# Optimization experiments

Hardware: AMD Instinct MI355X
Metric: run time of the kernel (lower is better)

Reference implementation:

```python
import jax, jax.numpy as jnp
import numpy as np

ATTN, ENC, DEC = 1024, 1024, 1024
B, S = 64, 2048

def setup_inputs() -> dict:
    key = jax.random.key(0)
    k1, k2, k3, k4, k5, k6 = jax.random.split(key, 6)
    sc_w = 1.0 / np.sqrt(ENC + DEC)
    sc_v = 1.0 / np.sqrt(ATTN)
    return {
        "hidden": jax.random.normal(k1, (B, DEC), dtype=jnp.float32),
        "vectors_to_attend": jax.random.normal(k2, (S, B, ENC), dtype=jnp.float32),
        "attn_w_weight": jax.random.uniform(k3, (ATTN, ENC + DEC), jnp.float32, -sc_w, sc_w),
        "attn_w_bias": jax.random.uniform(k4, (ATTN,), jnp.float32, -sc_w, sc_w),
        "attn_v_weight": jax.random.uniform(k5, (1, ATTN), jnp.float32, -sc_v, sc_v),
        "attn_v_bias": jax.random.uniform(k6, (1,), jnp.float32, -sc_v, sc_v),
    }

def reference(hidden, vectors_to_attend, attn_w_weight, attn_w_bias, attn_v_weight, attn_v_bias):
    # vectors_to_attend: [S, B, E] -> [B, S, E]
    v = jnp.transpose(vectors_to_attend, (1, 0, 2))
    # Split attn_w over the concat dim: concat([v, h]) @ W^T == v @ We^T + h @ Wd^T
    We = attn_w_weight[:, :ENC]   # [A, E]
    Wd = attn_w_weight[:, ENC:]   # [A, D]
    # energies: [B, S, A]
    e = jnp.tanh(jnp.einsum('bse,ae->bsa', v, We)
                 + jnp.einsum('bd,ad->ba', hidden, Wd)[:, None, :]
                 + attn_w_bias)
    # scores: [B, S]
    scores = jnp.einsum('bsa,a->bs', e, attn_v_weight[0]) + attn_v_bias[0]
    weights = jax.nn.softmax(scores, axis=1)          # softmax over seq dim
    context = jnp.einsum('bs,bse->be', weights, v)    # [B, E]
    return context[:, None, :]                        # [B, 1, E] to match bmm output
```

## Files before the change

### kernel.cpp

```cpp
#include <hip/hip_runtime.h>
#include <hip/hip_bf16.h>
#include <math.h>

#define BB 64
#define SS 2048
#define MT (SS*BB)
#define NT 16

typedef __attribute__((ext_vector_type(4))) float f4;
typedef __attribute__((ext_vector_type(8))) short s8;

__device__ __forceinline__ unsigned short f2bf(float x) {
  union { float f; unsigned u; } v; v.f = x;
  unsigned r = v.u + 0x7FFFu + ((v.u >> 16) & 1u);
  return (unsigned short)(r >> 16);
}
__device__ __forceinline__ float bf2f(unsigned short x) {
  union { unsigned u; float f; } v; v.u = ((unsigned)x) << 16;
  return v.f;
}
__device__ __forceinline__ float fast_tanh(float x) {
  float t = __expf(2.0f * x);
  return 1.0f - 2.0f * __builtin_amdgcn_rcpf(t + 1.0f);
}

#define GLD16(gp, lp) __builtin_amdgcn_global_load_lds( \
    (const __attribute__((address_space(1))) void*)(gp), \
    (__attribute__((address_space(3))) void*)(lp), 16, 0, 0)
#define WAITV4() asm volatile("s_waitcnt vmcnt(4)" ::: "memory")
#define WAITV2() asm volatile("s_waitcnt vmcnt(2)" ::: "memory")
#define WAITV0() asm volatile("s_waitcnt vmcnt(0)" ::: "memory")
#define BAR()    __builtin_amdgcn_s_barrier()

__global__ void k_pack(const float* __restrict__ src, unsigned short* __restrict__ dst,
                       int stride) {
  __shared__ float ls[64][260];
  int g = blockIdx.x, cb = blockIdx.y, tid = threadIdx.x;
  int cl = (tid & 63) * 4, rbk = tid >> 6;
  const float* s0 = src + (size_t)(g * 64) * stride + cb * 256 + cl;
  #pragma unroll
  for (int it = 0; it < 16; ++it) {
    int rr = it * 4 + rbk;
    *(f4*)&ls[rr][cl] = *(const f4*)(s0 + (size_t)rr * stride);
  }
  __syncthreads();
  int kt_l = tid >> 6;
  int rr = tid & 63;
  int kt = cb * 4 + kt_l;
  int grow = g * 64 + rr;
  int panel = grow >> 8, pr = grow & 255, h = pr >> 7, r = pr & 127;
  unsigned short* d = dst + (((size_t)panel * 16 + kt) * 2 + h) * 8192 + r * 64;
  int rx = r & 7;
  #pragma unroll
  for (int sp = 0; sp < 8; ++sp) {
    const float* q = &ls[rr][kt_l * 64 + ((sp ^ rx) * 8)];
    f4 x0 = *(const f4*)q, x1 = *(const f4*)(q + 4);
    s8 o;
    #pragma unroll
    for (int j = 0; j < 4; ++j) { o[j] = (short)f2bf(x0[j]); o[4 + j] = (short)f2bf(x1[j]); }
    *(s8*)(d + sp * 8) = o;
  }
}

__global__ void k_hp(const float* __restrict__ hidden, const float* __restrict__ w,
                     const float* __restrict__ wbias, float* __restrict__ hp) {
  __shared__ float hs[1024];
  int b = blockIdx.x, tid = threadIdx.x;
  for (int i = tid; i < 1024; i += 256) hs[i] = hidden[b * 1024 + i];
  __syncthreads();
  int a = blockIdx.y * 256 + tid;
  const f4* wd = (const f4*)(w + a * 2048 + 1024);
  const f4* hv = (const f4*)hs;
  float acc = wbias[a];
  #pragma unroll 8
  for (int d = 0; d < 256; ++d) {
    f4 x = wd[d], y = hv[d];
    acc += x[0]*y[0] + x[1]*y[1] + x[2]*y[2] + x[3]*y[3];
  }
  hp[b * 1024 + a] = acc;
}

__global__ __launch_bounds__(512, 2) void k_gemm(
    const unsigned short* __restrict__ Avbs, const unsigned short* __restrict__ Wbs,
    const float* __restrict__ hp, const float* __restrict__ vw,
    float* __restrict__ part, int bm0, int nbm) {
  extern __shared__ char smem[];
  int bid = blockIdx.x;
  int nwg = nbm * 4;
  int wg = bid;
  if ((nwg & 7) == 0) { int cpx = nwg >> 3; wg = (bid & 7) * cpx + (bid >> 3); }
  int bn = wg & 3;
  int bmL = wg >> 2;
  int tid = threadIdx.x, lane = tid & 63;
  int wid = tid >> 6, wr = wid >> 2, wc = wid & 3;
  int c = lane & 15, kq = lane >> 4;

  int sx0 = ((kq) ^ (c & 7)) << 4;
  int sx1 = ((4 + kq) ^ (c & 7)) << 4;
  int aoff = wr * 16384 + c * 128;
  int boff = 32768 + (wc >> 1) * 16384 + ((wc & 1) * 64 + c) * 128;

  const unsigned short* Abase = Avbs + (size_t)bmL * 262144 + tid * 8;
  const unsigned short* Bbase = Wbs + (size_t)bn * 262144 + tid * 8;
  auto stage = [&](int tt, int u) {
    char* d = smem + (tt & 1) * 65536 + u * 16384 + tid * 16;
    const unsigned short* s = ((u & 2) ? Bbase : Abase) + ((size_t)tt * 2 + (u & 1)) * 8192;
    GLD16(s, d);
    GLD16(s + 4096, d + 8192);
  };

  f4 acc[8][4];
  f4 z = {0.f, 0.f, 0.f, 0.f};
  #pragma unroll
  for (int i = 0; i < 8; ++i)
    #pragma unroll
    for (int j = 0; j < 4; ++j) acc[i][j] = z;

  s8 va[4], vb0[4], vb1[4];

#define LDA(rb, mh, SX) { const char* ba_ = (rb) + aoff + (mh) * 8192 + (SX); \
    va[0] = *(const s8*)(ba_); va[1] = *(const s8*)(ba_ + 2048); \
    va[2] = *(const s8*)(ba_ + 4096); va[3] = *(const s8*)(ba_ + 6144); }
#define LDB(rb, VB, SX) { const char* bb_ = (rb) + boff + (SX); \
    VB[0] = *(const s8*)(bb_); VB[1] = *(const s8*)(bb_ + 2048); \
    VB[2] = *(const s8*)(bb_ + 4096); VB[3] = *(const s8*)(bb_ + 6144); }
#define MM(mh, VB) { \
    __builtin_amdgcn_s_setprio(1); \
    _Pragma("unroll") \
    for (int m_ = 0; m_ < 4; ++m_) { \
      acc[(mh)*4+m_][0] = __builtin_amdgcn_mfma_f32_16x16x32_bf16(va[m_], VB[0], acc[(mh)*4+m_][0], 0, 0, 0); \
      acc[(mh)*4+m_][1] = __builtin_amdgcn_mfma_f32_16x16x32_bf16(va[m_], VB[1], acc[(mh)*4+m_][1], 0, 0, 0); \
      acc[(mh)*4+m_][2] = __builtin_amdgcn_mfma_f32_16x16x32_bf16(va[m_], VB[2], acc[(mh)*4+m_][2], 0, 0, 0); \
      acc[(mh)*4+m_][3] = __builtin_amdgcn_mfma_f32_16x16x32_bf16(va[m_], VB[3], acc[(mh)*4+m_][3], 0, 0, 0); \
    } \
    __builtin_amdgcn_s_setprio(0); }

  stage(0, 0); stage(0, 1); stage(0, 2); stage(0, 3);
  stage(1, 2); stage(1, 3);
  WAITV4();
  BAR();

  #pragma unroll 1
  for (int t = 0; t < NT; ++t) {
    const char* rb = smem + (t & 1) * 65536;
    LDA(rb, 0, sx0); LDB(rb, vb0, sx0);
    if (t < 15) stage(t + 1, 0);
    BAR();
    MM(0, vb0);
    BAR();
    LDA(rb, 0, sx1); LDB(rb, vb1, sx1);
    if (t < 15) stage(t + 1, 1);
    BAR();
    MM(0, vb1);
    BAR();
    LDA(rb, 1, sx0);
    if (t < 14) stage(t + 2, 2);
    BAR();
    MM(1, vb0);
    BAR();
    LDA(rb, 1, sx1);
    if (t < 14) stage(t + 2, 3);
    BAR();
    MM(1, vb1);
    if (t < 14) WAITV2();
    else if (t == 14) WAITV0();
    BAR();
  }
#undef LDA
#undef LDB
#undef MM

  int lg = kq;
  int bm = bm0 + bmL;
  float rs[8][4];
  #pragma unroll
  for (int mi = 0; mi < 8; ++mi)
    #pragma unroll
    for (int j = 0; j < 4; ++j) rs[mi][j] = 0.f;
  #pragma unroll
  for (int ni = 0; ni < 4; ++ni) {
    int a_col = bn * 256 + wc * 64 + ni * 16 + c;
    float vwa = vw[a_col];
    const float* hpa = hp + a_col;
    #pragma unroll
    for (int mi = 0; mi < 8; ++mi) {
      #pragma unroll
      for (int j = 0; j < 4; ++j) {
        int r = wr * 128 + mi * 16 + lg * 4 + j;
        int b = r & 63;
        float x = acc[mi][ni][j] + hpa[b * 1024];
        rs[mi][j] += fast_tanh(x) * vwa;
      }
    }
  }
  #pragma unroll
  for (int off = 1; off < 16; off <<= 1) {
    #pragma unroll
    for (int mi = 0; mi < 8; ++mi)
      #pragma unroll
      for (int j = 0; j < 4; ++j)
        rs[mi][j] += __shfl_xor(rs[mi][j], off, 64);
  }
  if (c == 0) {
    int p = bn * 4 + wc;
    #pragma unroll
    for (int mi = 0; mi < 8; ++mi)
      #pragma unroll
      for (int j = 0; j < 4; ++j) {
        int m = bm * 256 + wr * 128 + mi * 16 + lg * 4 + j;
        int b = m & 63, s = m >> 6;
        part[(size_t)p * MT + b * SS + s] = rs[mi][j];
      }
  }
}

__global__ void k_softmax(const float* __restrict__ part, float* __restrict__ wt) {
  int b = blockIdx.x, tid = threadIdx.x, lane = tid & 63, wid = tid >> 6;
  __shared__ float red[8];
  float sc[8];
  float mx = -1e30f;
  #pragma unroll
  for (int i = 0; i < 8; ++i) {
    int s = tid + i * 256;
    float a = 0.f;
    #pragma unroll
    for (int p = 0; p < 16; ++p) a += part[(size_t)p * MT + b * SS + s];
    sc[i] = a; mx = fmaxf(mx, a);
  }
  for (int o = 1; o < 64; o <<= 1) mx = fmaxf(mx, __shfl_xor(mx, o, 64));
  if (lane == 0) red[wid] = mx;
  __syncthreads();
  mx = fmaxf(fmaxf(red[0], red[1]), fmaxf(red[2], red[3]));
  float sum = 0.f;
  #pragma unroll
  for (int i = 0; i < 8; ++i) { sc[i] = expf(sc[i] - mx); sum += sc[i]; }
  for (int o = 1; o < 64; o <<= 1) sum += __shfl_xor(sum, o, 64);
  if (lane == 0) red[4 + wid] = sum;
  __syncthreads();
  sum = red[4] + red[5] + red[6] + red[7];
  float inv = 1.f / sum;
  #pragma unroll
  for (int i = 0; i < 8; ++i) wt[b * SS + tid + i * 256] = sc[i] * inv;
}

__global__ void k_ctx_bfs(const unsigned short* __restrict__ vbs, const float* __restrict__ wt,
                          float* __restrict__ ctxp) {
  int b = blockIdx.x, cch = blockIdx.y, tid = threadIdx.x;
  int e = tid * 4;
  int kt = e >> 6, sl = (e >> 3) & 7, off = e & 7;
  f4 acc = {0.f, 0.f, 0.f, 0.f};
  int s0 = cch * 128;
  const float* wrow = wt + b * SS;
  #pragma unroll 4
  for (int s = s0; s < s0 + 128; ++s) {
    float ws = wrow[s];
    int row = s * 64 + b;
    int panel = row >> 8, pr = row & 255, h = pr >> 7, r = pr & 127;
    size_t addr = (((size_t)panel * 16 + kt) * 2 + h) * 8192 + r * 64 + ((sl ^ (r & 7)) << 3) + off;
    ushort4 u = *(const ushort4*)(vbs + addr);
    acc[0] += bf2f(u.x) * ws;
    acc[1] += bf2f(u.y) * ws;
    acc[2] += bf2f(u.z) * ws;
    acc[3] += bf2f(u.w) * ws;
  }
  *(f4*)(ctxp + (size_t)(cch * 64 + b) * 1024 + tid * 4) = acc;
}

__global__ void k_ctx_f32(const float* __restrict__ v, const float* __restrict__ wt,
                          float* __restrict__ ctxp) {
  int b = blockIdx.x, cch = blockIdx.y, tid = threadIdx.x;
  f4 acc = {0.f, 0.f, 0.f, 0.f};
  int s0 = cch * 128;
  const float* wrow = wt + b * SS;
  #pragma unroll 4
  for (int s = s0; s < s0 + 128; ++s) {
    float ws = wrow[s];
    const f4* vp = (const f4*)(v + (size_t)(s * 64 + b) * 1024);
    acc += vp[tid] * ws;
  }
  *(f4*)(ctxp + (size_t)(cch * 64 + b) * 1024 + tid * 4) = acc;
}

__global__ void k_out(const float* __restrict__ ctxp, float* __restrict__ out) {
  int b = blockIdx.x, tid = threadIdx.x;
  f4 acc = {0.f, 0.f, 0.f, 0.f};
  #pragma unroll
  for (int cch = 0; cch < 16; ++cch)
    acc += *(const f4*)(ctxp + (size_t)(cch * 64 + b) * 1024 + tid * 4);
  *(f4*)(out + b * 1024 + tid * 4) = acc;
}

extern "C" void kernel_launch(void* const* d_in, const int* in_sizes, int n_in,
                              void* d_out, int out_size, void* d_ws, size_t ws_size,
                              hipStream_t stream) {
  const float* hidden = (const float*)d_in[0];
  const float* v      = (const float*)d_in[1];
  const float* ww     = (const float*)d_in[2];
  const float* wbias  = (const float*)d_in[3];
  const float* vwgt   = (const float*)d_in[4];
  float* out = (float*)d_out;

  char* ws = (char*)d_ws;
  float*          hp   = (float*)(ws);
  unsigned short* wbs  = (unsigned short*)(ws + 262144);
  float*          part = (float*)(ws + 262144 + 2097152);
  float*          wt   = (float*)(ws + 262144 + 2097152 + 8388608);
  float*          ctxp = (float*)(ws + 262144 + 2097152 + 8388608 + 524288);
  size_t fixed = 262144 + 2097152 + 8388608 + 524288 + 4194304;
  unsigned short* vbs  = (unsigned short*)(ws + fixed);

  size_t avail = (ws_size > fixed) ? (ws_size - fixed) : 0;
  long rows_chunk = (long)(avail / 2048) & ~511L;
  if (rows_chunk > MT) rows_chunk = MT;
  if (rows_chunk < 512) rows_chunk = 512;
  int nchunks = (int)((MT + rows_chunk - 1) / rows_chunk);

  hipFuncSetAttribute((const void*)k_gemm, hipFuncAttributeMaxDynamicSharedMemorySize, 131072);

  k_pack<<<dim3(16, 4), 256, 0, stream>>>(ww, wbs, 2048);
  k_hp<<<dim3(64, 4), 256, 0, stream>>>(hidden, ww, wbias, hp);

  for (long r0 = 0; r0 < MT; r0 += rows_chunk) {
    long nr = MT - r0; if (nr > rows_chunk) nr = rows_chunk;
    int nbm = (int)(nr / 256);
    k_pack<<<dim3((int)(nr / 64), 4), 256, 0, stream>>>(v + (size_t)r0 * 1024, vbs, 1024);
    k_gemm<<<nbm * 4, 512, 131072, stream>>>(vbs, wbs, hp, vwgt, part, (int)(r0 / 256), nbm);
  }

  k_softmax<<<64, 256, 0, stream>>>(part, wt);
  if (nchunks == 1)
    k_ctx_bfs<<<dim3(64, 16), 256, 0, stream>>>(vbs, wt, ctxp);
  else
    k_ctx_f32<<<dim3(64, 16), 256, 0, stream>>>(v, wt, ctxp);
  k_out<<<64, 256, 0, stream>>>(ctxp, out);
}
```

Baseline: 586.6 us.

## Load GEMM B operand directly from global, halve LDS, stage hp in LDS

The W operand is no longer staged through LDS; each wave reads its B fragments straight from global/L2 into registers, prefetching one K-step ahead. Only A is double-buffered in LDS, which halves dynamic shared memory from 128KB to 64KB and cuts the number of barriers per K iteration. The epilogue first copies the block's slice of the hidden projection into LDS so the bias add no longer does strided global reads. The trade-off is that every wave issues more global loads for W, which relies on L2 hits, and the wait counts have to stay correct under the new load ordering.

```diff
diff --git a/kernel.cpp b/kernel.cpp
--- a/kernel.cpp
+++ b/kernel.cpp
@@ -28,8 +28,6 @@
     (const __attribute__((address_space(1))) void*)(gp), \
     (__attribute__((address_space(3))) void*)(lp), 16, 0, 0)
 #define WAITV4() asm volatile("s_waitcnt vmcnt(4)" ::: "memory")
-#define WAITV2() asm volatile("s_waitcnt vmcnt(2)" ::: "memory")
-#define WAITV0() asm volatile("s_waitcnt vmcnt(0)" ::: "memory")
 #define BAR()    __builtin_amdgcn_s_barrier()
 
 __global__ void k_pack(const float* __restrict__ src, unsigned short* __restrict__ dst,
@@ -97,14 +95,22 @@
 
   int sx0 = ((kq) ^ (c & 7)) << 4;
   int sx1 = ((4 + kq) ^ (c & 7)) << 4;
-  int aoff = wr * 16384 + c * 128;
-  int boff = 32768 + (wc >> 1) * 16384 + ((wc & 1) * 64 + c) * 128;
+  int sxe0 = sx0 >> 1, sxe1 = sx1 >> 1;
+
+  const unsigned short* Bt = Wbs + (size_t)bn * 262144;
+  int nrb = wc * 64 + c;
+  const unsigned short* Bp0 = Bt + ((nrb >> 7) * 8192 + (nrb & 127) * 64);
+  int nr1 = nrb + 16;
+  const unsigned short* Bp1 = Bt + ((nr1 >> 7) * 8192 + (nr1 & 127) * 64);
+  int nr2 = nrb + 32;
+  const unsigned short* Bp2 = Bt + ((nr2 >> 7) * 8192 + (nr2 & 127) * 64);
+  int nr3 = nrb + 48;
+  const unsigned short* Bp3 = Bt + ((nr3 >> 7) * 8192 + (nr3 & 127) * 64);
 
   const unsigned short* Abase = Avbs + (size_t)bmL * 262144 + tid * 8;
-  const unsigned short* Bbase = Wbs + (size_t)bn * 262144 + tid * 8;
-  auto stage = [&](int tt, int u) {
-    char* d = smem + (tt & 1) * 65536 + u * 16384 + tid * 16;
-    const unsigned short* s = ((u & 2) ? Bbase : Abase) + ((size_t)tt * 2 + (u & 1)) * 8192;
+  auto stageA = [&](int tt, int h) {
+    char* d = smem + (tt & 1) * 32768 + h * 16384 + tid * 16;
+    const unsigned short* s = Abase + ((size_t)tt * 2 + h) * 8192;
     GLD16(s, d);
     GLD16(s + 4096, d + 8192);
   };
@@ -116,59 +122,69 @@
     #pragma unroll
     for (int j = 0; j < 4; ++j) acc[i][j] = z;
 
-  s8 va[4], vb0[4], vb1[4];
-
-#define LDA(rb, mh, SX) { const char* ba_ = (rb) + aoff + (mh) * 8192 + (SX); \
-    va[0] = *(const s8*)(ba_); va[1] = *(const s8*)(ba_ + 2048); \
-    va[2] = *(const s8*)(ba_ + 4096); va[3] = *(const s8*)(ba_ + 6144); }
-#define LDB(rb, VB, SX) { const char* bb_ = (rb) + boff + (SX); \
-    VB[0] = *(const s8*)(bb_); VB[1] = *(const s8*)(bb_ + 2048); \
-    VB[2] = *(const s8*)(bb_ + 4096); VB[3] = *(const s8*)(bb_ + 6144); }
-#define MM(mh, VB) { \
+  s8 vaA[4], vaB[4], vb0[4], vb1[4];
+
+#define LDSA(DST, BASE, SX) { const char* p_ = (BASE) + (SX); \
+    DST[0] = *(const s8*)(p_);        DST[1] = *(const s8*)(p_ + 2048); \
+    DST[2] = *(const s8*)(p_ + 4096); DST[3] = *(const s8*)(p_ + 6144); }
+#define LDB4(DST, TOFF, SXE) { \
+    DST[0] = *(const s8*)(Bp0 + (TOFF) + (SXE)); \
+    DST[1] = *(const s8*)(Bp1 + (TOFF) + (SXE)); \
+    DST[2] = *(const s8*)(Bp2 + (TOFF) + (SXE)); \
+    DST[3] = *(const s8*)(Bp3 + (TOFF) + (SXE)); }
+#define MM(mh, VA, VB) { \
     __builtin_amdgcn_s_setprio(1); \
     _Pragma("unroll") \
     for (int m_ = 0; m_ < 4; ++m_) { \
-      acc[(mh)*4+m_][0] = __builtin_amdgcn_mfma_f32_16x16x32_bf16(va[m_], VB[0], acc[(mh)*4+m_][0], 0, 0, 0); \
-      acc[(mh)*4+m_][1] = __builtin_amdgcn_mfma_f32_16x16x32_bf16(va[m_], VB[1], acc[(mh)*4+m_][1], 0, 0, 0); \
-      acc[(mh)*4+m_][2] = __builtin_amdgcn_mfma_f32_16x16x32_bf16(va[m_], VB[2], acc[(mh)*4+m_][2], 0, 0, 0); \
-      acc[(mh)*4+m_][3] = __builtin_amdgcn_mfma_f32_16x16x32_bf16(va[m_], VB[3], acc[(mh)*4+m_][3], 0, 0, 0); \
+      acc[(mh)*4+m_][0] = __builtin_amdgcn_mfma_f32_16x16x32_bf16(VA[m_], VB[0], acc[(mh)*4+m_][0], 0, 0, 0); \
+      acc[(mh)*4+m_][1] = __builtin_amdgcn_mfma_f32_16x16x32_bf16(VA[m_], VB[1], acc[(mh)*4+m_][1], 0, 0, 0); \
+      acc[(mh)*4+m_][2] = __builtin_amdgcn_mfma_f32_16x16x32_bf16(VA[m_], VB[2], acc[(mh)*4+m_][2], 0, 0, 0); \
+      acc[(mh)*4+m_][3] = __builtin_amdgcn_mfma_f32_16x16x32_bf16(VA[m_], VB[3], acc[(mh)*4+m_][3], 0, 0, 0); \
     } \
     __builtin_amdgcn_s_setprio(0); }
 
-  stage(0, 0); stage(0, 1); stage(0, 2); stage(0, 3);
-  stage(1, 2); stage(1, 3);
+  stageA(0, 0); stageA(0, 1);
+  LDB4(vb0, 0, sxe0);
   WAITV4();
   BAR();
 
   #pragma unroll 1
   for (int t = 0; t < NT; ++t) {
-    const char* rb = smem + (t & 1) * 65536;
-    LDA(rb, 0, sx0); LDB(rb, vb0, sx0);
-    if (t < 15) stage(t + 1, 0);
+    const char* bufb = smem + (t & 1) * 32768 + wr * 16384 + c * 128;
+    LDSA(vaA, bufb, sx0);
+    LDSA(vaB, bufb + 8192, sx0);
+    if (t < 15) stageA(t + 1, 0);
+    LDB4(vb1, t * 16384, sxe1);
+    MM(0, vaA, vb0);
     BAR();
-    MM(0, vb0);
+    LDSA(vaA, bufb, sx1);
+    if (t < 15) stageA(t + 1, 1);
+    MM(1, vaB, vb0);
     BAR();
-    LDA(rb, 0, sx1); LDB(rb, vb1, sx1);
-    if (t < 15) stage(t + 1, 1);
+    LDSA(vaB, bufb + 8192, sx1);
+    if (t < 15) LDB4(vb0, (t + 1) * 16384, sxe0);
+    MM(0, vaA, vb1);
     BAR();
-    MM(0, vb1);
+    WAITV4();
+    MM(1, vaB, vb1);
     BAR();
-    LDA(rb, 1, sx0);
-    if (t < 14) stage(t + 2, 2);
-    BAR();
-    MM(1, vb0);
-    BAR();
-    LDA(rb, 1, sx1);
-    if (t < 14) stage(t + 2, 3);
-    BAR();
-    MM(1, vb1);
-    if (t < 14) WAITV2();
-    else if (t == 14) WAITV0();
-    BAR();
-  }
-#undef LDA
-#undef LDB
+  }
+#undef LDSA
+#undef LDB4
 #undef MM
+
+  {
+    const float* hprow = hp + bn * 256;
+    float* lhp = (float*)smem;
+    #pragma unroll
+    for (int qd = 0; qd < 8; ++qd) {
+      int i = qd * 512 + tid;
+      int b = i >> 6, col4 = i & 63;
+      *(f4*)(lhp + b * 256 + col4 * 4) = *(const f4*)(hprow + (size_t)b * 1024 + col4 * 4);
+    }
+  }
+  __syncthreads();
+  const float* lhpf = (const float*)smem;
 
   int lg = kq;
   int bm = bm0 + bmL;
@@ -179,16 +195,15 @@
     for (int j = 0; j < 4; ++j) rs[mi][j] = 0.f;
   #pragma unroll
   for (int ni = 0; ni < 4; ++ni) {
-    int a_col = bn * 256 + wc * 64 + ni * 16 + c;
-    float vwa = vw[a_col];
-    const float* hpa = hp + a_col;
+    int colL = wc * 64 + ni * 16 + c;
+    float vwa = vw[bn * 256 + colL];
     #pragma unroll
     for (int mi = 0; mi < 8; ++mi) {
       #pragma unroll
       for (int j = 0; j < 4; ++j) {
         int r = wr * 128 + mi * 16 + lg * 4 + j;
         int b = r & 63;
-        float x = acc[mi][ni][j] + hpa[b * 1024];
+        float x = acc[mi][ni][j] + lhpf[b * 256 + colL];
         rs[mi][j] += fast_tanh(x) * vwa;
       }
     }
@@ -315,7 +330,7 @@
   if (rows_chunk < 512) rows_chunk = 512;
   int nchunks = (int)((MT + rows_chunk - 1) / rows_chunk);
 
-  hipFuncSetAttribute((const void*)k_gemm, hipFuncAttributeMaxDynamicSharedMemorySize, 131072);
+  hipFuncSetAttribute((const void*)k_gemm, hipFuncAttributeMaxDynamicSharedMemorySize, 65536);
 
   k_pack<<<dim3(16, 4), 256, 0, stream>>>(ww, wbs, 2048);
   k_hp<<<dim3(64, 4), 256, 0, stream>>>(hidden, ww, wbias, hp);
@@ -324,7 +339,7 @@
     long nr = MT - r0; if (nr > rows_chunk) nr = rows_chunk;
     int nbm = (int)(nr / 256);
     k_pack<<<dim3((int)(nr / 64), 4), 256, 0, stream>>>(v + (size_t)r0 * 1024, vbs, 1024);
-    k_gemm<<<nbm * 4, 512, 131072, stream>>>(vbs, wbs, hp, vwgt, part, (int)(r0 / 256), nbm);
+    k_gemm<<<nbm * 4, 512, 65536, stream>>>(vbs, wbs, hp, vwgt, part, (int)(r0 / 256), nbm);
   }
 
   k_softmax<<<64, 256, 0, stream>>>(part, wt);
```

After: 682.7 us. 16.4% more time.
